# Kernel optimization log

Measured on AMD Instinct MI355X. Metric: run time of the kernel, lower is better.

Reference implementation:

```python
import jax, jax.numpy as jnp
import numpy as np

B, S, H, I, E, K = 4, 2048, 1024, 4096, 8, 2


def setup_inputs() -> dict:
    key = jax.random.key(0)
    ks = jax.random.split(key, 6)
    x = jax.random.normal(ks[0], (B, S, H), dtype=jnp.float32)
    gate_w = jax.random.normal(ks[1], (H, E), dtype=jnp.float32) * 0.02
    up_w = jax.random.normal(ks[2], (E, H, I), dtype=jnp.float32) * 0.02
    up_b = jnp.zeros((E, I), dtype=jnp.float32)
    down_w = jax.random.normal(ks[3], (E, I, H), dtype=jnp.float32) * 0.02
    down_b = jnp.zeros((E, H), dtype=jnp.float32)
    return {"x": x, "gate_w": gate_w, "up_w": up_w, "up_b": up_b,
            "down_w": down_w, "down_b": down_b}


def reference(x, gate_w, up_w, up_b, down_w, down_b):
    # Router: logits [B,S,E], softmax probs
    logits = jnp.einsum('bsh,he->bse', x, gate_w)
    probs = jax.nn.softmax(logits, axis=-1)
    # top-k selection and renormalization of the selected probabilities
    topk_p, topk_idx = jax.lax.top_k(probs, K)            # [B,S,K]
    topk_p = topk_p / jnp.sum(topk_p, axis=-1, keepdims=True)
    # combine weights per expert: [B,S,E] (sum of renormalized top-k probs routed to e)
    combine = jnp.sum(jax.nn.one_hot(topk_idx, E, dtype=x.dtype) * topk_p[..., None], axis=2)
    # per-expert FFN, weighted combine (loop over fixed small expert set)
    out = jnp.zeros_like(x)
    for e in range(E):
        h = jax.nn.gelu(jnp.einsum('bsh,hi->bsi', x, up_w[e]) + up_b[e], approximate=False)
        y = jnp.einsum('bsi,ih->bsh', h, down_w[e]) + down_b[e]
        out = out + combine[..., e:e + 1] * y
    # aux statistics
    expert_usage = jnp.mean(probs, axis=(0, 1))           # [E]
    load_balance_loss = E * jnp.sum(expert_usage * expert_usage)
    top_expert = topk_idx[..., 0]                          # [B,S]
    return out, load_balance_loss, expert_usage, top_expert
```

## Files before the change

kernel.cpp:

```cpp
#include <hip/hip_runtime.h>
#include <cmath>

#define T_TOK 8192
#define HDIM 1024
#define IDIM 4096
#define NEXP 8

#define OFF_LOSS  8388608
#define OFF_USAGE 8388609
#define OFF_TOPE  8388617

typedef __attribute__((ext_vector_type(8))) short bf16x8;
typedef __attribute__((ext_vector_type(4))) float f32x4;
typedef unsigned short u16;
typedef unsigned int u32;

__device__ inline u16 f2bf(float f) {
  u32 u = __float_as_uint(f);
  u32 r = (u + 0x7FFFu + ((u >> 16) & 1u)) >> 16;
  return (u16)r;
}

__device__ inline void glds16(const void* g, void* l) {
  __builtin_amdgcn_global_load_lds(
      (const __attribute__((address_space(1))) u32*)g,
      (__attribute__((address_space(3))) u32*)l, 16, 0, 0);
}

__global__ __launch_bounds__(256)
void cvt_x(const float* __restrict__ x, u16* __restrict__ xb) {
  size_t i = ((size_t)blockIdx.x * 256 + threadIdx.x) * 8;
  float4 a = *(const float4*)(x + i);
  float4 b = *(const float4*)(x + i + 4);
  union { u16 s[8]; uint4 v; } u;
  u.s[0] = f2bf(a.x); u.s[1] = f2bf(a.y); u.s[2] = f2bf(a.z); u.s[3] = f2bf(a.w);
  u.s[4] = f2bf(b.x); u.s[5] = f2bf(b.y); u.s[6] = f2bf(b.z); u.s[7] = f2bf(b.w);
  *(uint4*)(xb + i) = u.v;
}

__global__ __launch_bounds__(256)
void transpose_cvt64(const float* __restrict__ src, u16* __restrict__ dst, int R, int C) {
  __shared__ float tile[64][65];
  size_t eoff = (size_t)blockIdx.z * R * C;
  int r0 = blockIdx.y * 64, c0 = blockIdx.x * 64;
  const float* s = src + eoff;
  u16* d = dst + eoff;
  int tr = threadIdx.x >> 4;
  int tc = (threadIdx.x & 15) * 4;
#pragma unroll
  for (int it = 0; it < 4; it++) {
    int row = tr + it * 16;
    float4 v = *(const float4*)(s + (size_t)(r0 + row) * C + c0 + tc);
    tile[row][tc] = v.x; tile[row][tc + 1] = v.y;
    tile[row][tc + 2] = v.z; tile[row][tc + 3] = v.w;
  }
  __syncthreads();
  int wc = threadIdx.x >> 3;
  int wr = (threadIdx.x & 7) * 8;
#pragma unroll
  for (int it = 0; it < 2; it++) {
    int c = wc + it * 32;
    union { u16 s[8]; uint4 v; } u;
#pragma unroll
    for (int j = 0; j < 8; j++) u.s[j] = f2bf(tile[wr + j][c]);
    *(uint4*)(d + (size_t)(c0 + c) * R + r0 + wr) = u.v;
  }
}

__global__ __launch_bounds__(256)
void router_kernel(const float* __restrict__ x, const float* __restrict__ gw,
                   float* __restrict__ probs, int* __restrict__ counts,
                   int* __restrict__ tlist, float* __restrict__ wlist,
                   float* __restrict__ out) {
  int wid = threadIdx.x >> 6, lane = threadIdx.x & 63;
  int tok = blockIdx.x * 4 + wid;
  double acc[NEXP];
#pragma unroll
  for (int e = 0; e < NEXP; e++) acc[e] = 0.0;
  const float* xr = x + (size_t)tok * HDIM;
  for (int h = lane; h < HDIM; h += 64) {
    double xv = (double)xr[h];
    const float* g = gw + h * NEXP;
#pragma unroll
    for (int e = 0; e < NEXP; e++) acc[e] += xv * (double)g[e];
  }
#pragma unroll
  for (int off = 32; off > 0; off >>= 1) {
#pragma unroll
    for (int e = 0; e < NEXP; e++) acc[e] += __shfl_xor(acc[e], off);
  }
  if (lane == 0) {
    double m = acc[0];
#pragma unroll
    for (int e = 1; e < NEXP; e++) if (acc[e] > m) m = acc[e];
    double p[NEXP], ssum = 0.0;
#pragma unroll
    for (int e = 0; e < NEXP; e++) { p[e] = exp(acc[e] - m); ssum += p[e]; }
#pragma unroll
    for (int e = 0; e < NEXP; e++) p[e] /= ssum;
    int i1 = 0;
#pragma unroll
    for (int e = 1; e < NEXP; e++) if (p[e] > p[i1]) i1 = e;
    int i2 = (i1 == 0) ? 1 : 0;
#pragma unroll
    for (int e = 0; e < NEXP; e++) if (e != i1 && p[e] > p[i2]) i2 = e;
    double ps = p[i1] + p[i2];
#pragma unroll
    for (int e = 0; e < NEXP; e++) probs[(size_t)tok * NEXP + e] = (float)p[e];
    out[OFF_TOPE + tok] = (float)i1;
    int pos1 = atomicAdd(&counts[i1], 1);
    tlist[i1 * T_TOK + pos1] = tok;
    wlist[i1 * T_TOK + pos1] = (float)(p[i1] / ps);
    int pos2 = atomicAdd(&counts[i2], 1);
    tlist[i2 * T_TOK + pos2] = tok;
    wlist[i2 * T_TOK + pos2] = (float)(p[i2] / ps);
  }
}

__global__ void hbase_kernel(const int* __restrict__ counts, int* __restrict__ hbase) {
  if (threadIdx.x == 0 && blockIdx.x == 0) {
    int s = 0;
    for (int e = 0; e < NEXP; e++) { hbase[e] = s; s += counts[e]; }
    hbase[NEXP] = s;
  }
}

__global__ __launch_bounds__(256)
void usage_kernel(const float* __restrict__ probs, float* __restrict__ out) {
  int e = blockIdx.x;
  float s = 0.f;
  for (int t = threadIdx.x; t < T_TOK; t += 256) s += probs[(size_t)t * NEXP + e];
#pragma unroll
  for (int off = 32; off > 0; off >>= 1) s += __shfl_xor(s, off);
  __shared__ float red[4];
  int lane = threadIdx.x & 63, wid = threadIdx.x >> 6;
  if (lane == 0) red[wid] = s;
  __syncthreads();
  if (threadIdx.x == 0)
    out[OFF_USAGE + e] = (red[0] + red[1] + red[2] + red[3]) / (float)T_TOK;
}

__global__ void loss_kernel(float* __restrict__ out) {
  if (threadIdx.x == 0 && blockIdx.x == 0) {
    float s = 0.f;
    for (int e = 0; e < NEXP; e++) { float u = out[OFF_USAGE + e]; s += u * u; }
    out[OFF_LOSS] = (float)NEXP * s;
  }
}


__global__ __launch_bounds__(256, 3)
void up_gemm(const u16* __restrict__ xb, const u16* __restrict__ wbt,
             const float* __restrict__ bias, const int* __restrict__ counts,
             const int* __restrict__ hbase, const int* __restrict__ tlist,
             u16* __restrict__ hout, int e_fixed) {
  const int NT = IDIM / 128;
  const int MT = T_TOK / 128;
  int q = gridDim.x >> 3;
  int orig = blockIdx.x;
  int wg = (orig & 7) * q + (orig >> 3);
  int e, tm, tn;
  if (e_fixed >= 0) { e = e_fixed; tm = wg / NT; tn = wg % NT; }
  else { e = wg / (MT * NT); int r = wg % (MT * NT); tm = r / NT; tn = r % NT; }
  int cnt = counts[e];
  int m0 = tm * 128;
  if (m0 >= cnt) return;
  int hb = (e_fixed >= 0) ? 0 : hbase[e];
  int n0 = tn * 128;

  __shared__ u16 As[2 * 4096];
  __shared__ u16 Bs[2 * 4096];

  int t = threadIdx.x;
  int ra = t >> 2;
  int sw = (t & 3) ^ ((ra >> 1) & 3);

  const int* tl = tlist + e * T_TOK;
  int g0 = m0 + ra;      if (g0 > cnt - 1) g0 = cnt - 1;
  int g1 = m0 + ra + 64; if (g1 > cnt - 1) g1 = cnt - 1;
  const u16* pa0 = xb + (size_t)tl[g0] * HDIM + sw * 8;
  const u16* pa1 = xb + (size_t)tl[g1] * HDIM + sw * 8;
  const u16* wb = wbt + (size_t)e * IDIM * HDIM;
  const u16* pb0 = wb + (size_t)(n0 + ra) * HDIM + sw * 8;
  const u16* pb1 = wb + (size_t)(n0 + ra + 64) * HDIM + sw * 8;

  f32x4 acc[4][4];
#pragma unroll
  for (int i = 0; i < 4; i++)
#pragma unroll
    for (int j = 0; j < 4; j++) acc[i][j] = (f32x4){0.f, 0.f, 0.f, 0.f};

  int lane = t & 63, wid = t >> 6;
  int wr = (wid >> 1) * 64, wc = (wid & 1) * 64;
  int lrow = lane & 15, lslot = lane >> 4;

  auto stage = [&](int b, int k0) {
    u16* a = &As[b * 4096];
    u16* bb = &Bs[b * 4096];
    glds16(pa0 + k0, a + t * 8);
    glds16(pa1 + k0, a + 2048 + t * 8);
    glds16(pb0 + k0, bb + t * 8);
    glds16(pb1 + k0, bb + 2048 + t * 8);
  };
  auto compute = [&](int b) {
    const u16* A = &As[b * 4096];
    const u16* Bb = &Bs[b * 4096];
    bf16x8 af[4], bfv[4];
#pragma unroll
    for (int mi = 0; mi < 4; mi++) {
      int row = wr + mi * 16 + lrow;
      af[mi] = *(const bf16x8*)&A[row * 32 + ((lslot ^ ((row >> 1) & 3)) * 8)];
    }
#pragma unroll
    for (int ni = 0; ni < 4; ni++) {
      int row = wc + ni * 16 + lrow;
      bfv[ni] = *(const bf16x8*)&Bb[row * 32 + ((lslot ^ ((row >> 1) & 3)) * 8)];
    }
#pragma unroll
    for (int mi = 0; mi < 4; mi++)
#pragma unroll
      for (int ni = 0; ni < 4; ni++)
        acc[mi][ni] = __builtin_amdgcn_mfma_f32_16x16x32_bf16(af[mi], bfv[ni], acc[mi][ni], 0, 0, 0);
  };

  const int nk = HDIM / 32;
  stage(0, 0);
  for (int kt = 0; kt < nk; ++kt) {
    int b = kt & 1;
    __builtin_amdgcn_s_barrier();
    if (kt + 1 < nk) {
      stage(b ^ 1, (kt + 1) * 32);
      asm volatile("s_waitcnt vmcnt(4)" ::: "memory");
    } else {
      asm volatile("s_waitcnt vmcnt(0)" ::: "memory");
    }
    compute(b);
  }

  float bv[4];
#pragma unroll
  for (int ni = 0; ni < 4; ni++)
    bv[ni] = bias[(size_t)e * IDIM + n0 + wc + ni * 16 + lrow];
  int r4 = lslot * 4;
#pragma unroll
  for (int mi = 0; mi < 4; mi++) {
    int rb = m0 + wr + mi * 16 + r4;
#pragma unroll
    for (int j = 0; j < 4; j++) {
      int row = rb + j;
      if (row < cnt) {
        u16* hp = hout + (size_t)(hb + row) * IDIM + n0 + wc + lrow;
#pragma unroll
        for (int ni = 0; ni < 4; ni++) {
          float v = acc[mi][ni][j] + bv[ni];
          float gl = 0.5f * v * (1.0f + erff(v * 0.70710678118654752f));
          hp[ni * 16] = f2bf(gl);
        }
      }
    }
  }
}

__global__ __launch_bounds__(256, 3)
void down_gemm(const u16* __restrict__ h, const u16* __restrict__ wbt,
               const float* __restrict__ bias, const int* __restrict__ counts,
               const int* __restrict__ hbase, const int* __restrict__ tlist,
               const float* __restrict__ wlist, float* __restrict__ out, int e_fixed) {
  const int NT = HDIM / 128;
  const int MT = T_TOK / 128;
  const int KS = 2;
  int q = gridDim.x >> 3;
  int orig = blockIdx.x;
  int wg = (orig & 7) * q + (orig >> 3);
  int e, r;
  if (e_fixed >= 0) { e = e_fixed; r = wg; }
  else { e = wg / (MT * NT * KS); r = wg % (MT * NT * KS); }
  int tm = r / (NT * KS);
  int r2 = r % (NT * KS);
  int ks = r2 / NT;
  int tn = r2 % NT;
  int cnt = counts[e];
  int m0 = tm * 128;
  if (m0 >= cnt) return;
  int hb = (e_fixed >= 0) ? 0 : hbase[e];
  int n0 = tn * 128;
  int kbase = ks * (IDIM / KS);

  __shared__ u16 As[2 * 4096];
  __shared__ u16 Bs[2 * 4096];

  int t = threadIdx.x;
  int ra = t >> 2;
  int sw = (t & 3) ^ ((ra >> 1) & 3);

  int g0 = m0 + ra;      if (g0 > cnt - 1) g0 = cnt - 1;
  int g1 = m0 + ra + 64; if (g1 > cnt - 1) g1 = cnt - 1;
  const u16* pa0 = h + (size_t)(hb + g0) * IDIM + sw * 8;
  const u16* pa1 = h + (size_t)(hb + g1) * IDIM + sw * 8;
  const u16* wb = wbt + (size_t)e * HDIM * IDIM;
  const u16* pb0 = wb + (size_t)(n0 + ra) * IDIM + sw * 8;
  const u16* pb1 = wb + (size_t)(n0 + ra + 64) * IDIM + sw * 8;

  f32x4 acc[4][4];
#pragma unroll
  for (int i = 0; i < 4; i++)
#pragma unroll
    for (int j = 0; j < 4; j++) acc[i][j] = (f32x4){0.f, 0.f, 0.f, 0.f};

  int lane = t & 63, wid = t >> 6;
  int wr = (wid >> 1) * 64, wc = (wid & 1) * 64;
  int lrow = lane & 15, lslot = lane >> 4;

  auto stage = [&](int b, int k0) {
    u16* a = &As[b * 4096];
    u16* bb = &Bs[b * 4096];
    glds16(pa0 + k0, a + t * 8);
    glds16(pa1 + k0, a + 2048 + t * 8);
    glds16(pb0 + k0, bb + t * 8);
    glds16(pb1 + k0, bb + 2048 + t * 8);
  };
  auto compute = [&](int b) {
    const u16* A = &As[b * 4096];
    const u16* Bb = &Bs[b * 4096];
    bf16x8 af[4], bfv[4];
#pragma unroll
    for (int mi = 0; mi < 4; mi++) {
      int row = wr + mi * 16 + lrow;
      af[mi] = *(const bf16x8*)&A[row * 32 + ((lslot ^ ((row >> 1) & 3)) * 8)];
    }
#pragma unroll
    for (int ni = 0; ni < 4; ni++) {
      int row = wc + ni * 16 + lrow;
      bfv[ni] = *(const bf16x8*)&Bb[row * 32 + ((lslot ^ ((row >> 1) & 3)) * 8)];
    }
#pragma unroll
    for (int mi = 0; mi < 4; mi++)
#pragma unroll
      for (int ni = 0; ni < 4; ni++)
        acc[mi][ni] = __builtin_amdgcn_mfma_f32_16x16x32_bf16(af[mi], bfv[ni], acc[mi][ni], 0, 0, 0);
  };

  const int nk = (IDIM / KS) / 32;
  stage(0, kbase);
  for (int kt = 0; kt < nk; ++kt) {
    int b = kt & 1;
    __builtin_amdgcn_s_barrier();
    if (kt + 1 < nk) {
      stage(b ^ 1, kbase + (kt + 1) * 32);
      asm volatile("s_waitcnt vmcnt(4)" ::: "memory");
    } else {
      asm volatile("s_waitcnt vmcnt(0)" ::: "memory");
    }
    compute(b);
  }

  float bv[4];
#pragma unroll
  for (int ni = 0; ni < 4; ni++)
    bv[ni] = (ks == 0) ? bias[(size_t)e * HDIM + n0 + wc + ni * 16 + lrow] : 0.0f;
  int r4 = lslot * 4;
#pragma unroll
  for (int mi = 0; mi < 4; mi++) {
    int rb = m0 + wr + mi * 16 + r4;
#pragma unroll
    for (int j = 0; j < 4; j++) {
      int row = rb + j;
      if (row < cnt) {
        int tok = tlist[e * T_TOK + row];
        float w = wlist[e * T_TOK + row];
        float* op = out + (size_t)tok * HDIM + n0 + wc + lrow;
#pragma unroll
        for (int ni = 0; ni < 4; ni++)
          atomicAdd(&op[ni * 16], w * (acc[mi][ni][j] + bv[ni]));
      }
    }
  }
}

extern "C" void kernel_launch(void* const* d_in, const int* in_sizes, int n_in,
                              void* d_out, int out_size, void* d_ws, size_t ws_size,
                              hipStream_t stream) {
  const float* x   = (const float*)d_in[0];
  const float* gw  = (const float*)d_in[1];
  const float* upw = (const float*)d_in[2];
  const float* upb = (const float*)d_in[3];
  const float* dnw = (const float*)d_in[4];
  const float* dnb = (const float*)d_in[5];
  float* out = (float*)d_out;
  char* ws = (char*)d_ws;

  int*   counts = (int*)(ws + 0);
  int*   hbase  = (int*)(ws + 64);
  int*   tlist  = (int*)(ws + 256);
  float* wlist  = (float*)(ws + 256 + 262144);
  float* probs  = (float*)(ws + 256 + 2 * 262144);
  u16*   xb     = (u16*)(ws + 1048576);
  u16*   upbt   = (u16*)(ws + 1048576 + 16777216);
  u16*   dnbt   = (u16*)(ws + 1048576 + 16777216 + 67108864ull);
  u16*   hbuf   = (u16*)(ws + 1048576 + 16777216 + 2ull * 67108864ull);

  bool grouped = ws_size >= 286261248ull;

  hipMemsetAsync(counts, 0, 32, stream);
  hipMemsetAsync(d_out, 0, (size_t)out_size * 4, stream);

  cvt_x<<<4096, 256, 0, stream>>>(x, xb);
  transpose_cvt64<<<dim3(IDIM / 64, HDIM / 64, NEXP), 256, 0, stream>>>(upw, upbt, HDIM, IDIM);
  transpose_cvt64<<<dim3(HDIM / 64, IDIM / 64, NEXP), 256, 0, stream>>>(dnw, dnbt, IDIM, HDIM);
  router_kernel<<<T_TOK / 4, 256, 0, stream>>>(x, gw, probs, counts, tlist, wlist, out);
  hbase_kernel<<<1, 64, 0, stream>>>(counts, hbase);
  usage_kernel<<<NEXP, 256, 0, stream>>>(probs, out);
  loss_kernel<<<1, 64, 0, stream>>>(out);

  if (grouped) {
    up_gemm<<<NEXP * 64 * 32, 256, 0, stream>>>(xb, upbt, upb, counts, hbase, tlist, hbuf, -1);
    down_gemm<<<NEXP * 64 * 8 * 2, 256, 0, stream>>>(hbuf, dnbt, dnb, counts, hbase, tlist, wlist, out, -1);
  } else {
    for (int e = 0; e < NEXP; e++) {
      up_gemm<<<64 * 32, 256, 0, stream>>>(xb, upbt, upb, counts, hbase, tlist, hbuf, e);
      down_gemm<<<64 * 8 * 2, 256, 0, stream>>>(hbuf, dnbt, dnb, counts, hbase, tlist, wlist, out, e);
    }
  }
}
```

Measured before the change: 768.0 us.

## Use 256x256 GEMM tiles with 8 waves and split A/B staging

Both expert GEMMs move from 128x128 tiles with 4 waves to 256x256 tiles with 8 waves per block. Each wave computes two 64-row halves that reuse the same B fragments, so global traffic per FLOP drops. A and B loads are staged at different points in the iteration, and s_setprio is raised around the MFMA bursts to overlap loads with compute. The cost is more barriers per k-step, more accumulator registers, double the LDS, and coarser tiles that waste more work on partially filled expert tiles.

```diff
diff --git a/kernel.cpp b/kernel.cpp
--- a/kernel.cpp
+++ b/kernel.cpp
@@ -149,13 +149,32 @@
 }
 
 
-__global__ __launch_bounds__(256, 3)
+#define GEMM_PREAMBLE                                                     \
+  int t = threadIdx.x;                                                    \
+  int rs = t >> 2;                       \
+  int swz = (t & 3) ^ ((rs >> 1) & 3);           \
+  int lane = t & 63, wid = t >> 6;                                        \
+  int lrow = lane & 15, lslot = lane >> 4;                                \
+  int whA = wid >> 2;                                     \
+  int wcB = (wid & 3) * 64;                      \
+  f32x4 acc[8][4];                                                        \
+  _Pragma("unroll") for (int i = 0; i < 8; i++)                           \
+  _Pragma("unroll") for (int j = 0; j < 4; j++)                           \
+      acc[i][j] = (f32x4){0.f, 0.f, 0.f, 0.f};
+
+__device__ __forceinline__ bf16x8 lds_read(const u16* base, int cur, int half,
+                                           int r1, int lslot) {
+  int sl = lslot ^ ((r1 >> 1) & 3);
+  return *(const bf16x8*)&base[cur * 8192 + half * 4096 + r1 * 32 + sl * 8];
+}
+
+__global__ __launch_bounds__(512, 2)
 void up_gemm(const u16* __restrict__ xb, const u16* __restrict__ wbt,
              const float* __restrict__ bias, const int* __restrict__ counts,
              const int* __restrict__ hbase, const int* __restrict__ tlist,
              u16* __restrict__ hout, int e_fixed) {
-  const int NT = IDIM / 128;
-  const int MT = T_TOK / 128;
+  const int NT = IDIM / 256;
+  const int MT = T_TOK / 256;
   int q = gridDim.x >> 3;
   int orig = blockIdx.x;
   int wg = (orig & 7) * q + (orig >> 3);
@@ -163,93 +182,92 @@
   if (e_fixed >= 0) { e = e_fixed; tm = wg / NT; tn = wg % NT; }
   else { e = wg / (MT * NT); int r = wg % (MT * NT); tm = r / NT; tn = r % NT; }
   int cnt = counts[e];
-  int m0 = tm * 128;
+  int m0 = tm * 256;
   if (m0 >= cnt) return;
   int hb = (e_fixed >= 0) ? 0 : hbase[e];
-  int n0 = tn * 128;
-
-  __shared__ u16 As[2 * 4096];
-  __shared__ u16 Bs[2 * 4096];
-
-  int t = threadIdx.x;
-  int ra = t >> 2;
-  int sw = (t & 3) ^ ((ra >> 1) & 3);
+  int n0 = tn * 256;
+
+  __shared__ u16 As[2 * 8192];
+  __shared__ u16 Bs[2 * 8192];
+
+  GEMM_PREAMBLE
 
   const int* tl = tlist + e * T_TOK;
-  int g0 = m0 + ra;      if (g0 > cnt - 1) g0 = cnt - 1;
-  int g1 = m0 + ra + 64; if (g1 > cnt - 1) g1 = cnt - 1;
-  const u16* pa0 = xb + (size_t)tl[g0] * HDIM + sw * 8;
-  const u16* pa1 = xb + (size_t)tl[g1] * HDIM + sw * 8;
+  int ga0 = m0 + rs;       if (ga0 > cnt - 1) ga0 = cnt - 1;
+  int ga1 = m0 + 128 + rs; if (ga1 > cnt - 1) ga1 = cnt - 1;
+  const u16* pa0 = xb + (size_t)tl[ga0] * HDIM + swz * 8;
+  const u16* pa1 = xb + (size_t)tl[ga1] * HDIM + swz * 8;
   const u16* wb = wbt + (size_t)e * IDIM * HDIM;
-  const u16* pb0 = wb + (size_t)(n0 + ra) * HDIM + sw * 8;
-  const u16* pb1 = wb + (size_t)(n0 + ra + 64) * HDIM + sw * 8;
-
-  f32x4 acc[4][4];
-#pragma unroll
-  for (int i = 0; i < 4; i++)
-#pragma unroll
-    for (int j = 0; j < 4; j++) acc[i][j] = (f32x4){0.f, 0.f, 0.f, 0.f};
-
-  int lane = t & 63, wid = t >> 6;
-  int wr = (wid >> 1) * 64, wc = (wid & 1) * 64;
-  int lrow = lane & 15, lslot = lane >> 4;
-
-  auto stage = [&](int b, int k0) {
-    u16* a = &As[b * 4096];
-    u16* bb = &Bs[b * 4096];
-    glds16(pa0 + k0, a + t * 8);
-    glds16(pa1 + k0, a + 2048 + t * 8);
-    glds16(pb0 + k0, bb + t * 8);
-    glds16(pb1 + k0, bb + 2048 + t * 8);
+  const u16* pb0 = wb + (size_t)(n0 + rs) * HDIM + swz * 8;
+  const u16* pb1 = wb + (size_t)(n0 + 128 + rs) * HDIM + swz * 8;
+
+  auto stageA = [&](int b, int kt) {
+    glds16(pa0 + kt * 32, &As[b * 8192 + t * 8]);
+    glds16(pa1 + kt * 32, &As[b * 8192 + 4096 + t * 8]);
   };
-  auto compute = [&](int b) {
-    const u16* A = &As[b * 4096];
-    const u16* Bb = &Bs[b * 4096];
-    bf16x8 af[4], bfv[4];
-#pragma unroll
-    for (int mi = 0; mi < 4; mi++) {
-      int row = wr + mi * 16 + lrow;
-      af[mi] = *(const bf16x8*)&A[row * 32 + ((lslot ^ ((row >> 1) & 3)) * 8)];
-    }
+  auto stageB = [&](int b, int kt) {
+    glds16(pb0 + kt * 32, &Bs[b * 8192 + t * 8]);
+    glds16(pb1 + kt * 32, &Bs[b * 8192 + 4096 + t * 8]);
+  };
+
+  const int nk = HDIM / 32;
+  stageA(0, 0); stageB(0, 0);
+  for (int kt = 0; kt < nk; ++kt) {
+    int cur = kt & 1;
+    if (kt + 1 < nk) {
+      stageA(cur ^ 1, kt + 1);
+      asm volatile("s_waitcnt vmcnt(2)" ::: "memory");
+    } else {
+      asm volatile("s_waitcnt vmcnt(0)" ::: "memory");
+    }
+    __builtin_amdgcn_s_barrier();
+    asm volatile("" ::: "memory");
+    bf16x8 bfv[4], af[4];
 #pragma unroll
     for (int ni = 0; ni < 4; ni++) {
-      int row = wc + ni * 16 + lrow;
-      bfv[ni] = *(const bf16x8*)&Bb[row * 32 + ((lslot ^ ((row >> 1) & 3)) * 8)];
-    }
+      int rB = wcB + ni * 16 + lrow;
+      bfv[ni] = lds_read(Bs, cur, rB >> 7, rB & 127, lslot);
+    }
+#pragma unroll
+    for (int mi = 0; mi < 4; mi++)
+      af[mi] = lds_read(As, cur, whA, mi * 16 + lrow, lslot);
+    __builtin_amdgcn_s_setprio(1);
 #pragma unroll
     for (int mi = 0; mi < 4; mi++)
 #pragma unroll
       for (int ni = 0; ni < 4; ni++)
         acc[mi][ni] = __builtin_amdgcn_mfma_f32_16x16x32_bf16(af[mi], bfv[ni], acc[mi][ni], 0, 0, 0);
-  };
-
-  const int nk = HDIM / 32;
-  stage(0, 0);
-  for (int kt = 0; kt < nk; ++kt) {
-    int b = kt & 1;
-    __builtin_amdgcn_s_barrier();
-    if (kt + 1 < nk) {
-      stage(b ^ 1, (kt + 1) * 32);
-      asm volatile("s_waitcnt vmcnt(4)" ::: "memory");
-    } else {
-      asm volatile("s_waitcnt vmcnt(0)" ::: "memory");
-    }
-    compute(b);
+    __builtin_amdgcn_s_setprio(0);
+    __builtin_amdgcn_s_barrier();
+    asm volatile("" ::: "memory");
+    if (kt + 1 < nk) stageB(cur ^ 1, kt + 1);
+#pragma unroll
+    for (int mi = 0; mi < 4; mi++)
+      af[mi] = lds_read(As, cur, whA, 64 + mi * 16 + lrow, lslot);
+    __builtin_amdgcn_s_setprio(1);
+#pragma unroll
+    for (int mi = 0; mi < 4; mi++)
+#pragma unroll
+      for (int ni = 0; ni < 4; ni++)
+        acc[4 + mi][ni] = __builtin_amdgcn_mfma_f32_16x16x32_bf16(af[mi], bfv[ni], acc[4 + mi][ni], 0, 0, 0);
+    __builtin_amdgcn_s_setprio(0);
+    __builtin_amdgcn_s_barrier();
+    asm volatile("" ::: "memory");
   }
 
   float bv[4];
 #pragma unroll
   for (int ni = 0; ni < 4; ni++)
-    bv[ni] = bias[(size_t)e * IDIM + n0 + wc + ni * 16 + lrow];
+    bv[ni] = bias[(size_t)e * IDIM + n0 + wcB + ni * 16 + lrow];
   int r4 = lslot * 4;
 #pragma unroll
-  for (int mi = 0; mi < 4; mi++) {
-    int rb = m0 + wr + mi * 16 + r4;
+  for (int mi = 0; mi < 8; mi++) {
+    int rb = m0 + whA * 128 + mi * 16 + r4;
 #pragma unroll
     for (int j = 0; j < 4; j++) {
       int row = rb + j;
       if (row < cnt) {
-        u16* hp = hout + (size_t)(hb + row) * IDIM + n0 + wc + lrow;
+        u16* hp = hout + (size_t)(hb + row) * IDIM + n0 + wcB + lrow;
 #pragma unroll
         for (int ni = 0; ni < 4; ni++) {
           float v = acc[mi][ni][j] + bv[ni];
@@ -261,13 +279,13 @@
   }
 }
 
-__global__ __launch_bounds__(256, 3)
+__global__ __launch_bounds__(512, 2)
 void down_gemm(const u16* __restrict__ h, const u16* __restrict__ wbt,
                const float* __restrict__ bias, const int* __restrict__ counts,
                const int* __restrict__ hbase, const int* __restrict__ tlist,
                const float* __restrict__ wlist, float* __restrict__ out, int e_fixed) {
-  const int NT = HDIM / 128;
-  const int MT = T_TOK / 128;
+  const int NT = HDIM / 256;
+  const int MT = T_TOK / 256;
   const int KS = 2;
   int q = gridDim.x >> 3;
   int orig = blockIdx.x;
@@ -280,95 +298,94 @@
   int ks = r2 / NT;
   int tn = r2 % NT;
   int cnt = counts[e];
-  int m0 = tm * 128;
+  int m0 = tm * 256;
   if (m0 >= cnt) return;
   int hb = (e_fixed >= 0) ? 0 : hbase[e];
-  int n0 = tn * 128;
+  int n0 = tn * 256;
   int kbase = ks * (IDIM / KS);
 
-  __shared__ u16 As[2 * 4096];
-  __shared__ u16 Bs[2 * 4096];
-
-  int t = threadIdx.x;
-  int ra = t >> 2;
-  int sw = (t & 3) ^ ((ra >> 1) & 3);
-
-  int g0 = m0 + ra;      if (g0 > cnt - 1) g0 = cnt - 1;
-  int g1 = m0 + ra + 64; if (g1 > cnt - 1) g1 = cnt - 1;
-  const u16* pa0 = h + (size_t)(hb + g0) * IDIM + sw * 8;
-  const u16* pa1 = h + (size_t)(hb + g1) * IDIM + sw * 8;
+  __shared__ u16 As[2 * 8192];
+  __shared__ u16 Bs[2 * 8192];
+
+  GEMM_PREAMBLE
+
+  int ga0 = m0 + rs;       if (ga0 > cnt - 1) ga0 = cnt - 1;
+  int ga1 = m0 + 128 + rs; if (ga1 > cnt - 1) ga1 = cnt - 1;
+  const u16* pa0 = h + (size_t)(hb + ga0) * IDIM + kbase + swz * 8;
+  const u16* pa1 = h + (size_t)(hb + ga1) * IDIM + kbase + swz * 8;
   const u16* wb = wbt + (size_t)e * HDIM * IDIM;
-  const u16* pb0 = wb + (size_t)(n0 + ra) * IDIM + sw * 8;
-  const u16* pb1 = wb + (size_t)(n0 + ra + 64) * IDIM + sw * 8;
-
-  f32x4 acc[4][4];
-#pragma unroll
-  for (int i = 0; i < 4; i++)
-#pragma unroll
-    for (int j = 0; j < 4; j++) acc[i][j] = (f32x4){0.f, 0.f, 0.f, 0.f};
-
-  int lane = t & 63, wid = t >> 6;
-  int wr = (wid >> 1) * 64, wc = (wid & 1) * 64;
-  int lrow = lane & 15, lslot = lane >> 4;
-
-  auto stage = [&](int b, int k0) {
-    u16* a = &As[b * 4096];
-    u16* bb = &Bs[b * 4096];
-    glds16(pa0 + k0, a + t * 8);
-    glds16(pa1 + k0, a + 2048 + t * 8);
-    glds16(pb0 + k0, bb + t * 8);
-    glds16(pb1 + k0, bb + 2048 + t * 8);
+  const u16* pb0 = wb + (size_t)(n0 + rs) * IDIM + kbase + swz * 8;
+  const u16* pb1 = wb + (size_t)(n0 + 128 + rs) * IDIM + kbase + swz * 8;
+
+  auto stageA = [&](int b, int kt) {
+    glds16(pa0 + kt * 32, &As[b * 8192 + t * 8]);
+    glds16(pa1 + kt * 32, &As[b * 8192 + 4096 + t * 8]);
   };
-  auto compute = [&](int b) {
-    const u16* A = &As[b * 4096];
-    const u16* Bb = &Bs[b * 4096];
-    bf16x8 af[4], bfv[4];
-#pragma unroll
-    for (int mi = 0; mi < 4; mi++) {
-      int row = wr + mi * 16 + lrow;
-      af[mi] = *(const bf16x8*)&A[row * 32 + ((lslot ^ ((row >> 1) & 3)) * 8)];
-    }
+  auto stageB = [&](int b, int kt) {
+    glds16(pb0 + kt * 32, &Bs[b * 8192 + t * 8]);
+    glds16(pb1 + kt * 32, &Bs[b * 8192 + 4096 + t * 8]);
+  };
+
+  const int nk = (IDIM / KS) / 32;
+  stageA(0, 0); stageB(0, 0);
+  for (int kt = 0; kt < nk; ++kt) {
+    int cur = kt & 1;
+    if (kt + 1 < nk) {
+      stageA(cur ^ 1, kt + 1);
+      asm volatile("s_waitcnt vmcnt(2)" ::: "memory");
+    } else {
+      asm volatile("s_waitcnt vmcnt(0)" ::: "memory");
+    }
+    __builtin_amdgcn_s_barrier();
+    asm volatile("" ::: "memory");
+    bf16x8 bfv[4], af[4];
 #pragma unroll
     for (int ni = 0; ni < 4; ni++) {
-      int row = wc + ni * 16 + lrow;
-      bfv[ni] = *(const bf16x8*)&Bb[row * 32 + ((lslot ^ ((row >> 1) & 3)) * 8)];
-    }
+      int rB = wcB + ni * 16 + lrow;
+      bfv[ni] = lds_read(Bs, cur, rB >> 7, rB & 127, lslot);
+    }
+#pragma unroll
+    for (int mi = 0; mi < 4; mi++)
+      af[mi] = lds_read(As, cur, whA, mi * 16 + lrow, lslot);
+    __builtin_amdgcn_s_setprio(1);
 #pragma unroll
     for (int mi = 0; mi < 4; mi++)
 #pragma unroll
       for (int ni = 0; ni < 4; ni++)
         acc[mi][ni] = __builtin_amdgcn_mfma_f32_16x16x32_bf16(af[mi], bfv[ni], acc[mi][ni], 0, 0, 0);
-  };
-
-  const int nk = (IDIM / KS) / 32;
-  stage(0, kbase);
-  for (int kt = 0; kt < nk; ++kt) {
-    int b = kt & 1;
-    __builtin_amdgcn_s_barrier();
-    if (kt + 1 < nk) {
-      stage(b ^ 1, kbase + (kt + 1) * 32);
-      asm volatile("s_waitcnt vmcnt(4)" ::: "memory");
-    } else {
-      asm volatile("s_waitcnt vmcnt(0)" ::: "memory");
-    }
-    compute(b);
+    __builtin_amdgcn_s_setprio(0);
+    __builtin_amdgcn_s_barrier();
+    asm volatile("" ::: "memory");
+    if (kt + 1 < nk) stageB(cur ^ 1, kt + 1);
+#pragma unroll
+    for (int mi = 0; mi < 4; mi++)
+      af[mi] = lds_read(As, cur, whA, 64 + mi * 16 + lrow, lslot);
+    __builtin_amdgcn_s_setprio(1);
+#pragma unroll
+    for (int mi = 0; mi < 4; mi++)
+#pragma unroll
+      for (int ni = 0; ni < 4; ni++)
+        acc[4 + mi][ni] = __builtin_amdgcn_mfma_f32_16x16x32_bf16(af[mi], bfv[ni], acc[4 + mi][ni], 0, 0, 0);
+    __builtin_amdgcn_s_setprio(0);
+    __builtin_amdgcn_s_barrier();
+    asm volatile("" ::: "memory");
   }
 
   float bv[4];
 #pragma unroll
   for (int ni = 0; ni < 4; ni++)
-    bv[ni] = (ks == 0) ? bias[(size_t)e * HDIM + n0 + wc + ni * 16 + lrow] : 0.0f;
+    bv[ni] = (ks == 0) ? bias[(size_t)e * HDIM + n0 + wcB + ni * 16 + lrow] : 0.0f;
   int r4 = lslot * 4;
 #pragma unroll
-  for (int mi = 0; mi < 4; mi++) {
-    int rb = m0 + wr + mi * 16 + r4;
+  for (int mi = 0; mi < 8; mi++) {
+    int rb = m0 + whA * 128 + mi * 16 + r4;
 #pragma unroll
     for (int j = 0; j < 4; j++) {
       int row = rb + j;
       if (row < cnt) {
         int tok = tlist[e * T_TOK + row];
         float w = wlist[e * T_TOK + row];
-        float* op = out + (size_t)tok * HDIM + n0 + wc + lrow;
+        float* op = out + (size_t)tok * HDIM + n0 + wcB + lrow;
 #pragma unroll
         for (int ni = 0; ni < 4; ni++)
           atomicAdd(&op[ni * 16], w * (acc[mi][ni][j] + bv[ni]));
@@ -413,12 +430,12 @@
   loss_kernel<<<1, 64, 0, stream>>>(out);
 
   if (grouped) {
-    up_gemm<<<NEXP * 64 * 32, 256, 0, stream>>>(xb, upbt, upb, counts, hbase, tlist, hbuf, -1);
-    down_gemm<<<NEXP * 64 * 8 * 2, 256, 0, stream>>>(hbuf, dnbt, dnb, counts, hbase, tlist, wlist, out, -1);
+    up_gemm<<<NEXP * 32 * 16, 512, 0, stream>>>(xb, upbt, upb, counts, hbase, tlist, hbuf, -1);
+    down_gemm<<<NEXP * 32 * 4 * 2, 512, 0, stream>>>(hbuf, dnbt, dnb, counts, hbase, tlist, wlist, out, -1);
   } else {
     for (int e = 0; e < NEXP; e++) {
-      up_gemm<<<64 * 32, 256, 0, stream>>>(xb, upbt, upb, counts, hbase, tlist, hbuf, e);
-      down_gemm<<<64 * 8 * 2, 256, 0, stream>>>(hbuf, dnbt, dnb, counts, hbase, tlist, wlist, out, e);
-    }
-  }
-}
+      up_gemm<<<32 * 16, 512, 0, stream>>>(xb, upbt, upb, counts, hbase, tlist, hbuf, e);
+      down_gemm<<<32 * 4 * 2, 512, 0, stream>>>(hbuf, dnbt, dnb, counts, hbase, tlist, wlist, out, e);
+    }
+  }
+}
```

New measurement: 979.5 us. 27.5% more time.
